# Kernel tuning notes

Measured on AMD Instinct MI355X. Metric: run time of the kernel, lower is better.

The kernel has to match this reference:

```python
import jax, jax.numpy as jnp
import numpy as np

N = 204800  # total nodes in the batched graph
B = 4096    # number of graphs (sessions)
D = 128     # embedding_dim


def setup_inputs() -> dict:
    key = jax.random.key(0)
    ks = jax.random.split(key, 10)
    feat_i = jax.random.normal(ks[0], (N, D), dtype=jnp.float32)
    U_feat = jax.random.normal(ks[1], (B, D), dtype=jnp.float32)
    # per-node click counts >= 1 so log(cnt) is finite
    cnt = jax.random.uniform(ks[2], (N,), dtype=jnp.float32, minval=1.0, maxval=50.0)
    scale = 1.0 / np.sqrt(D)
    W_key = jax.random.normal(ks[3], (D, D), dtype=jnp.float32) * scale
    W_user = jax.random.normal(ks[4], (D, D), dtype=jnp.float32) * scale
    b_user = jax.random.normal(ks[5], (D,), dtype=jnp.float32) * scale
    W_last = jax.random.normal(ks[6], (D, D), dtype=jnp.float32) * scale
    w_e = jax.random.normal(ks[7], (D, 1), dtype=jnp.float32) * scale
    last_nodes = jax.random.randint(ks[8], (B,), 0, N, dtype=jnp.int32)
    segment_ids = jnp.sort(jax.random.randint(ks[9], (N,), 0, B, dtype=jnp.int32))
    return {
        "feat_i": feat_i, "U_feat": U_feat, "cnt": cnt,
        "W_key": W_key, "W_user": W_user, "b_user": b_user,
        "W_last": W_last, "w_e": w_e,
        "last_nodes": last_nodes, "segment_ids": segment_ids,
    }


def reference(feat_i, U_feat, cnt, W_key, W_user, b_user, W_last, w_e,
              last_nodes, segment_ids):
    # linear projections (torch Linear y = x W^T + b; weights here are stored
    # pre-transposed so x @ W is the same math)
    feat_key = feat_i @ W_key                       # [N, D]
    U = U_feat @ W_user + b_user                    # [B, D]
    last_feat = feat_i[last_nodes] @ W_last         # [B, D]
    # dgl.broadcast_nodes: per-graph query replicated onto its nodes
    feat_qry = (U + last_feat)[segment_ids]         # [N, D]
    # additive-sigmoid attention score + log-count bias
    e = jax.nn.sigmoid(feat_qry + feat_key) @ w_e   # [N, 1]
    e = e + jnp.log(cnt)[:, None]                   # [N, 1]
    # segment softmax over ragged per-graph node segments
    m = jax.ops.segment_max(e, segment_ids, num_segments=B)      # [B, 1]
    ex = jnp.exp(e - m[segment_ids])                             # [N, 1]
    s = jax.ops.segment_sum(ex, segment_ids, num_segments=B)     # [B, 1]
    alpha = ex / s[segment_ids]                                  # [N, 1]
    # weighted segment reduce over raw node features (feat_val = feat_i)
    rst = jax.ops.segment_sum(alpha * feat_i, segment_ids, num_segments=B)  # [B, D]
    return rst
```

## Files before the change

### kernel.cpp

```cpp
#include <hip/hip_runtime.h>
#include <hip/hip_bf16.h>
#include <math.h>

#define N_NODES 204800
#define B_GRAPHS 4096
#define DIM 128

typedef __attribute__((ext_vector_type(8))) short bf16x8;
typedef __attribute__((ext_vector_type(4))) float f32x4;

__device__ __forceinline__ float sigf(float x) {
    return 1.0f / (1.0f + __expf(-x));
}

__device__ __forceinline__ unsigned short bfrne(float x) {
    unsigned u = __float_as_uint(x);
    unsigned r = u + 0x7FFFu + ((u >> 16) & 1u);
    return (unsigned short)(r >> 16);
}

__global__ __launch_bounds__(128) void qkernel(
    const float* __restrict__ feat, const float* __restrict__ U_feat,
    const float* __restrict__ W_user, const float* __restrict__ b_user,
    const float* __restrict__ W_last, const int* __restrict__ last_nodes,
    const float* __restrict__ W_key, unsigned short* __restrict__ Wt,
    const int* __restrict__ seg, int* __restrict__ bounds,
    float* __restrict__ q) {
  if (blockIdx.x >= 576) {
    int n = (blockIdx.x - 576) * 128 + threadIdx.x;
    int sc = seg[n];
    int sp = (n == 0) ? -1 : seg[n - 1];
    for (int b = sp + 1; b <= sc; ++b) bounds[b] = (b == 0) ? 0 : n;
    if (n == N_NODES - 1)
      for (int b = sc + 1; b <= B_GRAPHS; ++b) bounds[b] = N_NODES;
    return;
  }
  if (blockIdx.x >= 512) {
    int b = blockIdx.x - 512;
#pragma unroll
    for (int j = 0; j < 2; ++j) {
      int o = b * 256 + j * 128 + threadIdx.x;
      int c = o >> 7, k = o & 127;
      Wt[o] = bfrne(W_key[k * DIM + c]);
    }
    return;
  }
  __shared__ float sU[8][DIM];
  __shared__ float sL[8][DIM];
  const int d = threadIdx.x;
  const int g0 = blockIdx.x * 8;
  for (int g = 0; g < 8; ++g) {
    sU[g][d] = U_feat[(g0 + g) * DIM + d];
    int ln = last_nodes[g0 + g];
    sL[g][d] = feat[ln * DIM + d];
  }
  __syncthreads();
  float acc[8];
#pragma unroll
  for (int g = 0; g < 8; ++g) acc[g] = 0.0f;

  for (int kk = 0; kk < 32; ++kk) {
    float wu[4], wl[4];
#pragma unroll
    for (int j = 0; j < 4; ++j) {
      wu[j] = W_user[(kk * 4 + j) * DIM + d];
      wl[j] = W_last[(kk * 4 + j) * DIM + d];
    }
#pragma unroll
    for (int g = 0; g < 8; ++g) {
      float4 u4 = reinterpret_cast<const float4*>(sU[g])[kk];
      float4 l4 = reinterpret_cast<const float4*>(sL[g])[kk];
      acc[g] += u4.x * wu[0] + u4.y * wu[1] + u4.z * wu[2] + u4.w * wu[3];
      acc[g] += l4.x * wl[0] + l4.y * wl[1] + l4.z * wl[2] + l4.w * wl[3];
    }
  }
  float bu = b_user[d];
  for (int g = 0; g < 8; ++g) q[(g0 + g) * DIM + d] = acc[g] + bu;
}

__global__ __launch_bounds__(256, 2) void ekernel(
    const float* __restrict__ feat, const unsigned short* __restrict__ Wt,
    const float* __restrict__ w_e, const float* __restrict__ cnt,
    const int* __restrict__ seg, const float* __restrict__ q,
    float* __restrict__ e) {
  __shared__ unsigned short sW[128 * DIM];
  __shared__ float sWe[DIM];
  const int tid = threadIdx.x;
  const int base = blockIdx.x * 128;
  const int l = tid & 63, w = tid >> 6;
  const int lr = l & 15, lh = l >> 4;

  int sg[2];
#pragma unroll
  for (int t = 0; t < 2; ++t) sg[t] = seg[base + w * 32 + t * 16 + lr];

  float4 fv[2][4][2];
#pragma unroll
  for (int t = 0; t < 2; ++t) {
    const float* rp =
        feat + (size_t)(base + w * 32 + t * 16 + lr) * DIM + lh * 8;
#pragma unroll
    for (int ks = 0; ks < 4; ++ks) {
      fv[t][ks][0] = *reinterpret_cast<const float4*>(rp + ks * 32);
      fv[t][ks][1] = *reinterpret_cast<const float4*>(rp + ks * 32 + 4);
    }
  }

  const float4* q4p = reinterpret_cast<const float4*>(q);
  float4 qv[2][8];
#pragma unroll
  for (int t = 0; t < 2; ++t)
#pragma unroll
    for (int c = 0; c < 8; ++c)
      qv[t][c] = q4p[(size_t)sg[t] * 32 + c * 4 + lh];

  const uint4* Wt4 = reinterpret_cast<const uint4*>(Wt);
#pragma unroll
  for (int i = 0; i < 8; ++i) {
    int hw = i * 2048 + tid * 8;
    int row = hw >> 7, k0 = hw & 127;
    uint4 wv = Wt4[i * 256 + tid];
    *reinterpret_cast<uint4*>(&sW[row * DIM + (k0 ^ ((row & 7) << 3))]) = wv;
  }
  if (tid < 32)
    reinterpret_cast<float4*>(sWe)[tid] =
        reinterpret_cast<const float4*>(w_e)[tid];

  bf16x8 af[2][4];
#pragma unroll
  for (int t = 0; t < 2; ++t)
#pragma unroll
    for (int ks = 0; ks < 4; ++ks) {
      union { bf16x8 v; unsigned short u[8]; } a;
      a.u[0] = bfrne(fv[t][ks][0].x); a.u[1] = bfrne(fv[t][ks][0].y);
      a.u[2] = bfrne(fv[t][ks][0].z); a.u[3] = bfrne(fv[t][ks][0].w);
      a.u[4] = bfrne(fv[t][ks][1].x); a.u[5] = bfrne(fv[t][ks][1].y);
      a.u[6] = bfrne(fv[t][ks][1].z); a.u[7] = bfrne(fv[t][ks][1].w);
      af[t][ks] = a.v;
    }

  __syncthreads();

  float p0 = 0.0f, p1 = 0.0f;
#pragma unroll
  for (int c = 0; c < 8; ++c) {
    const int row = c * 16 + lr;
    bf16x8 wf[4];
#pragma unroll
    for (int ks = 0; ks < 4; ++ks)
      wf[ks] = *reinterpret_cast<const bf16x8*>(
          &sW[row * DIM + ((ks * 32 + lh * 8) ^ ((row & 7) << 3))]);
    float4 we = *reinterpret_cast<const float4*>(&sWe[c * 16 + lh * 4]);

    f32x4 a0 = f32x4{0.f, 0.f, 0.f, 0.f};
    f32x4 a1 = f32x4{0.f, 0.f, 0.f, 0.f};
#pragma unroll
    for (int ks = 0; ks < 4; ++ks) {
      a0 = __builtin_amdgcn_mfma_f32_16x16x32_bf16(wf[ks], af[0][ks], a0, 0, 0, 0);
      a1 = __builtin_amdgcn_mfma_f32_16x16x32_bf16(wf[ks], af[1][ks], a1, 0, 0, 0);
    }
    float4 q0 = qv[0][c], q1 = qv[1][c];
    p0 += we.x * sigf(a0[0] + q0.x) + we.y * sigf(a0[1] + q0.y) +
          we.z * sigf(a0[2] + q0.z) + we.w * sigf(a0[3] + q0.w);
    p1 += we.x * sigf(a1[0] + q1.x) + we.y * sigf(a1[1] + q1.y) +
          we.z * sigf(a1[2] + q1.z) + we.w * sigf(a1[3] + q1.w);
  }

  float pv[2] = {p0, p1};
#pragma unroll
  for (int t = 0; t < 2; ++t) {
    float v = pv[t];
    v += __shfl_xor(v, 16, 64);
    v += __shfl_xor(v, 32, 64);
    if (lh == 0) {
      int node = base + w * 32 + t * 16 + lr;
      e[node] = v + __logf(cnt[node]);
    }
  }
}

__global__ __launch_bounds__(256) void skernel(
    const float* __restrict__ feat, const int* __restrict__ bounds,
    float* __restrict__ e, float* __restrict__ rst) {
  const int b = blockIdx.x;
  const int tid = threadIdx.x;
  const int s0 = bounds[b];
  const int s1 = bounds[b + 1];

  if (s1 <= s0) {
    if (tid < DIM) rst[b * DIM + tid] = 0.0f;
    return;
  }

  __shared__ float red[8];
  __shared__ float part[8 * DIM];
  const int wave = tid >> 6, lane = tid & 63;

  float lm = -3.0e38f;
  for (int i = s0 + tid; i < s1; i += 256) lm = fmaxf(lm, e[i]);
#pragma unroll
  for (int off = 32; off >= 1; off >>= 1) lm = fmaxf(lm, __shfl_xor(lm, off, 64));
  if (lane == 0) red[wave] = lm;
  __syncthreads();
  const float m = fmaxf(fmaxf(red[0], red[1]), fmaxf(red[2], red[3]));

  float ls = 0.0f;
  for (int i = s0 + tid; i < s1; i += 256) {
    float p = __expf(e[i] - m);
    e[i] = p;
    ls += p;
  }
#pragma unroll
  for (int off = 32; off >= 1; off >>= 1) ls += __shfl_xor(ls, off, 64);
  if (lane == 0) red[4 + wave] = ls;
  __syncthreads();
  const float inv = 1.0f / (red[4] + red[5] + red[6] + red[7]);

  const int c = tid & 31;
  const int h = tid >> 5;
  float4 acc = float4{0.f, 0.f, 0.f, 0.f};
  const float4* feat4 = reinterpret_cast<const float4*>(feat);
  for (int n = s0 + h; n < s1; n += 8) {
    float p = e[n];
    float4 f = feat4[n * 32 + c];
    acc.x += p * f.x;
    acc.y += p * f.y;
    acc.z += p * f.z;
    acc.w += p * f.w;
  }
  reinterpret_cast<float4*>(part)[h * 32 + c] = acc;
  __syncthreads();
  if (tid < DIM) {
    float tot = 0.0f;
#pragma unroll
    for (int hh = 0; hh < 8; ++hh) tot += part[hh * DIM + tid];
    rst[b * DIM + tid] = tot * inv;
  }
}

extern "C" void kernel_launch(void* const* d_in, const int* in_sizes, int n_in,
                              void* d_out, int out_size, void* d_ws,
                              size_t ws_size, hipStream_t stream) {
  const float* feat = (const float*)d_in[0];
  const float* U_feat = (const float*)d_in[1];
  const float* cnt = (const float*)d_in[2];
  const float* W_key = (const float*)d_in[3];
  const float* W_user = (const float*)d_in[4];
  const float* b_user = (const float*)d_in[5];
  const float* W_last = (const float*)d_in[6];
  const float* w_e = (const float*)d_in[7];
  const int* last_nodes = (const int*)d_in[8];
  const int* seg = (const int*)d_in[9];
  float* out = (float*)d_out;

  float* q = (float*)d_ws;
  float* e = q + B_GRAPHS * DIM;
  unsigned short* Wt = (unsigned short*)(e + N_NODES);
  int* bounds = (int*)(Wt + DIM * DIM);

  qkernel<<<512 + 64 + N_NODES / 128, 128, 0, stream>>>(
      feat, U_feat, W_user, b_user, W_last, last_nodes, W_key, Wt, seg, bounds, q);
  ekernel<<<N_NODES / 128, 256, 0, stream>>>(feat, Wt, w_e, cnt, seg, q, e);
  skernel<<<B_GRAPHS, 256, 0, stream>>>(feat, bounds, e, out);
}
```

Baseline: 70.57 us.

## Process two node chunks per ekernel block and prefetch the second chunk's features

Each ekernel block now handles 256 nodes in two 128-node chunks instead of 128, which halves the number of times the 32 KB bf16 key weight is staged into shared memory. The second chunk's feature rows are loaded before the first chunk's MFMA and sigmoid work, so that global latency overlaps with compute. The cost is higher register pressure from a second feature buffer, and the occupancy hint of two blocks per CU has been dropped from launch bounds. The grid also shrinks to 800 blocks, which may reduce latency hiding.

```diff
diff --git a/kernel.cpp b/kernel.cpp
--- a/kernel.cpp
+++ b/kernel.cpp
@@ -78,7 +78,73 @@
   for (int g = 0; g < 8; ++g) q[(g0 + g) * DIM + d] = acc[g] + bu;
 }
 
-__global__ __launch_bounds__(256, 2) void ekernel(
+__device__ __forceinline__ void compute_chunk(
+    const unsigned short* sW, const float* sWe, const bf16x8 (&af)[2][4],
+    const float4 (&qv)[2][8], const float (&lc)[2], int nodebase, int lr,
+    int lh, float* __restrict__ e) {
+  float p[2] = {0.0f, 0.0f};
+#pragma unroll
+  for (int c = 0; c < 8; ++c) {
+    const int row = c * 16 + lr;
+    bf16x8 wf[4];
+#pragma unroll
+    for (int ks = 0; ks < 4; ++ks)
+      wf[ks] = *reinterpret_cast<const bf16x8*>(
+          &sW[row * DIM + ((ks * 32 + lh * 8) ^ ((row & 7) << 3))]);
+    float4 we = *reinterpret_cast<const float4*>(&sWe[c * 16 + lh * 4]);
+
+    f32x4 a0 = f32x4{0.f, 0.f, 0.f, 0.f};
+    f32x4 a1 = f32x4{0.f, 0.f, 0.f, 0.f};
+#pragma unroll
+    for (int ks = 0; ks < 4; ++ks) {
+      a0 = __builtin_amdgcn_mfma_f32_16x16x32_bf16(wf[ks], af[0][ks], a0, 0, 0, 0);
+      a1 = __builtin_amdgcn_mfma_f32_16x16x32_bf16(wf[ks], af[1][ks], a1, 0, 0, 0);
+    }
+    float4 q0 = qv[0][c], q1 = qv[1][c];
+    p[0] += we.x * sigf(a0[0] + q0.x) + we.y * sigf(a0[1] + q0.y) +
+            we.z * sigf(a0[2] + q0.z) + we.w * sigf(a0[3] + q0.w);
+    p[1] += we.x * sigf(a1[0] + q1.x) + we.y * sigf(a1[1] + q1.y) +
+            we.z * sigf(a1[2] + q1.z) + we.w * sigf(a1[3] + q1.w);
+  }
+#pragma unroll
+  for (int t = 0; t < 2; ++t) {
+    float v = p[t];
+    v += __shfl_xor(v, 16, 64);
+    v += __shfl_xor(v, 32, 64);
+    if (lh == 0) e[nodebase + t * 16 + lr] = v + __logf(lc[t]);
+  }
+}
+
+__device__ __forceinline__ void load_feat(const float* __restrict__ feat,
+                                          int node0, int lh, int lr,
+                                          float4 (&fv)[2][4][2]) {
+#pragma unroll
+  for (int t = 0; t < 2; ++t) {
+    const float* rp = feat + (size_t)(node0 + t * 16 + lr) * DIM + lh * 8;
+#pragma unroll
+    for (int ks = 0; ks < 4; ++ks) {
+      fv[t][ks][0] = *reinterpret_cast<const float4*>(rp + ks * 32);
+      fv[t][ks][1] = *reinterpret_cast<const float4*>(rp + ks * 32 + 4);
+    }
+  }
+}
+
+__device__ __forceinline__ void cvt_feat(const float4 (&fv)[2][4][2],
+                                         bf16x8 (&af)[2][4]) {
+#pragma unroll
+  for (int t = 0; t < 2; ++t)
+#pragma unroll
+    for (int ks = 0; ks < 4; ++ks) {
+      union { bf16x8 v; unsigned short u[8]; } a;
+      a.u[0] = bfrne(fv[t][ks][0].x); a.u[1] = bfrne(fv[t][ks][0].y);
+      a.u[2] = bfrne(fv[t][ks][0].z); a.u[3] = bfrne(fv[t][ks][0].w);
+      a.u[4] = bfrne(fv[t][ks][1].x); a.u[5] = bfrne(fv[t][ks][1].y);
+      a.u[6] = bfrne(fv[t][ks][1].z); a.u[7] = bfrne(fv[t][ks][1].w);
+      af[t][ks] = a.v;
+    }
+}
+
+__global__ __launch_bounds__(256) void ekernel(
     const float* __restrict__ feat, const unsigned short* __restrict__ Wt,
     const float* __restrict__ w_e, const float* __restrict__ cnt,
     const int* __restrict__ seg, const float* __restrict__ q,
@@ -86,25 +152,23 @@
   __shared__ unsigned short sW[128 * DIM];
   __shared__ float sWe[DIM];
   const int tid = threadIdx.x;
-  const int base = blockIdx.x * 128;
+  const int base0 = blockIdx.x * 256;
   const int l = tid & 63, w = tid >> 6;
   const int lr = l & 15, lh = l >> 4;
 
-  int sg[2];
-#pragma unroll
-  for (int t = 0; t < 2; ++t) sg[t] = seg[base + w * 32 + t * 16 + lr];
+  int sg[2][2];
+  float lc[2][2];
+#pragma unroll
+  for (int ch = 0; ch < 2; ++ch)
+#pragma unroll
+    for (int t = 0; t < 2; ++t) {
+      int node = base0 + ch * 128 + w * 32 + t * 16 + lr;
+      sg[ch][t] = seg[node];
+      lc[ch][t] = cnt[node];
+    }
 
   float4 fv[2][4][2];
-#pragma unroll
-  for (int t = 0; t < 2; ++t) {
-    const float* rp =
-        feat + (size_t)(base + w * 32 + t * 16 + lr) * DIM + lh * 8;
-#pragma unroll
-    for (int ks = 0; ks < 4; ++ks) {
-      fv[t][ks][0] = *reinterpret_cast<const float4*>(rp + ks * 32);
-      fv[t][ks][1] = *reinterpret_cast<const float4*>(rp + ks * 32 + 4);
-    }
-  }
+  load_feat(feat, base0 + w * 32, lh, lr, fv);
 
   const float4* q4p = reinterpret_cast<const float4*>(q);
   float4 qv[2][8];
@@ -112,7 +176,7 @@
   for (int t = 0; t < 2; ++t)
 #pragma unroll
     for (int c = 0; c < 8; ++c)
-      qv[t][c] = q4p[(size_t)sg[t] * 32 + c * 4 + lh];
+      qv[t][c] = q4p[(size_t)sg[0][t] * 32 + c * 4 + lh];
 
   const uint4* Wt4 = reinterpret_cast<const uint4*>(Wt);
 #pragma unroll
@@ -127,56 +191,22 @@
         reinterpret_cast<const float4*>(w_e)[tid];
 
   bf16x8 af[2][4];
+  cvt_feat(fv, af);
+
+  __syncthreads();
+
+  float4 fv2[2][4][2];
+  load_feat(feat, base0 + 128 + w * 32, lh, lr, fv2);
+
+  compute_chunk(sW, sWe, af, qv, lc[0], base0 + w * 32, lr, lh, e);
+
 #pragma unroll
   for (int t = 0; t < 2; ++t)
 #pragma unroll
-    for (int ks = 0; ks < 4; ++ks) {
-      union { bf16x8 v; unsigned short u[8]; } a;
-      a.u[0] = bfrne(fv[t][ks][0].x); a.u[1] = bfrne(fv[t][ks][0].y);
-      a.u[2] = bfrne(fv[t][ks][0].z); a.u[3] = bfrne(fv[t][ks][0].w);
-      a.u[4] = bfrne(fv[t][ks][1].x); a.u[5] = bfrne(fv[t][ks][1].y);
-      a.u[6] = bfrne(fv[t][ks][1].z); a.u[7] = bfrne(fv[t][ks][1].w);
-      af[t][ks] = a.v;
-    }
-
-  __syncthreads();
-
-  float p0 = 0.0f, p1 = 0.0f;
-#pragma unroll
-  for (int c = 0; c < 8; ++c) {
-    const int row = c * 16 + lr;
-    bf16x8 wf[4];
-#pragma unroll
-    for (int ks = 0; ks < 4; ++ks)
-      wf[ks] = *reinterpret_cast<const bf16x8*>(
-          &sW[row * DIM + ((ks * 32 + lh * 8) ^ ((row & 7) << 3))]);
-    float4 we = *reinterpret_cast<const float4*>(&sWe[c * 16 + lh * 4]);
-
-    f32x4 a0 = f32x4{0.f, 0.f, 0.f, 0.f};
-    f32x4 a1 = f32x4{0.f, 0.f, 0.f, 0.f};
-#pragma unroll
-    for (int ks = 0; ks < 4; ++ks) {
-      a0 = __builtin_amdgcn_mfma_f32_16x16x32_bf16(wf[ks], af[0][ks], a0, 0, 0, 0);
-      a1 = __builtin_amdgcn_mfma_f32_16x16x32_bf16(wf[ks], af[1][ks], a1, 0, 0, 0);
-    }
-    float4 q0 = qv[0][c], q1 = qv[1][c];
-    p0 += we.x * sigf(a0[0] + q0.x) + we.y * sigf(a0[1] + q0.y) +
-          we.z * sigf(a0[2] + q0.z) + we.w * sigf(a0[3] + q0.w);
-    p1 += we.x * sigf(a1[0] + q1.x) + we.y * sigf(a1[1] + q1.y) +
-          we.z * sigf(a1[2] + q1.z) + we.w * sigf(a1[3] + q1.w);
-  }
-
-  float pv[2] = {p0, p1};
-#pragma unroll
-  for (int t = 0; t < 2; ++t) {
-    float v = pv[t];
-    v += __shfl_xor(v, 16, 64);
-    v += __shfl_xor(v, 32, 64);
-    if (lh == 0) {
-      int node = base + w * 32 + t * 16 + lr;
-      e[node] = v + __logf(cnt[node]);
-    }
-  }
+    for (int c = 0; c < 8; ++c)
+      qv[t][c] = q4p[(size_t)sg[1][t] * 32 + c * 4 + lh];
+  cvt_feat(fv2, af);
+  compute_chunk(sW, sWe, af, qv, lc[1], base0 + 128 + w * 32, lr, lh, e);
 }
 
 __global__ __launch_bounds__(256) void skernel(
@@ -260,6 +290,6 @@
 
   qkernel<<<512 + 64 + N_NODES / 128, 128, 0, stream>>>(
       feat, U_feat, W_user, b_user, W_last, last_nodes, W_key, Wt, seg, bounds, q);
-  ekernel<<<N_NODES / 128, 256, 0, stream>>>(feat, Wt, w_e, cnt, seg, q, e);
+  ekernel<<<N_NODES / 256, 256, 0, stream>>>(feat, Wt, w_e, cnt, seg, q, e);
   skernel<<<B_GRAPHS, 256, 0, stream>>>(feat, bounds, e, out);
 }
```

Result: slower. 82.79 us (+17.3%).
